# Kernel tuning notes

Measured on AMD Instinct MI355X. Metric: run time of the kernel, lower is better.

## Reference

```python
import jax, jax.numpy as jnp
import numpy as np

B, TAU, D, DX, DZ, H = 512, 4, 5, 256, 16, 64
M = D * DZ
COEFF_KL = 1.0
LOG2PI = float(np.log(2.0 * np.pi))


def setup_inputs() -> dict:
    ks = jax.random.split(jax.random.key(0), 12)
    s = 0.05
    return {
        "x": jax.random.normal(ks[0], (B, TAU, D, DX), jnp.float32),
        "y": jax.random.normal(ks[1], (B, D, DX), jnp.float32),
        "mask_param": jnp.full((TAU, M, M), 5.0, jnp.float32),
        "w_enc": ((0.9 * jax.random.uniform(ks[2], (D, DZ, DX)) + 0.1) / DX).astype(jnp.float32),
        "w_dec": ((0.9 * jax.random.uniform(ks[3], (D, DX, DZ)) + 0.1) / DZ).astype(jnp.float32),
        "enc_W0": jax.random.normal(ks[4], (DZ, DX, H), jnp.float32) * s,
        "enc_b0": jnp.zeros((DZ, H), jnp.float32),
        "enc_W1": jax.random.normal(ks[5], (DZ, H), jnp.float32) * s,
        "enc_b1": jnp.zeros((DZ,), jnp.float32),
        "dec_W0": jax.random.normal(ks[6], (DX, DZ, H), jnp.float32) * s,
        "dec_b0": jnp.zeros((DX, H), jnp.float32),
        "dec_W1": jax.random.normal(ks[7], (DX, H), jnp.float32) * s,
        "dec_b1": jnp.zeros((DX,), jnp.float32),
        "t_W0": jax.random.normal(ks[8], (M, TAU * M, H), jnp.float32) * s,
        "t_b0": jnp.zeros((M, H), jnp.float32),
        "t_W1": jax.random.normal(ks[9], (M, H), jnp.float32) * s,
        "t_b1": jnp.zeros((M,), jnp.float32),
        "logvar_enc": jnp.full((D,), -1.0, jnp.float32),
        "logvar_dec": jnp.full((D,), -1.0, jnp.float32),
        "t_logvar": jnp.full((D, DZ), -4.0, jnp.float32),
    }


def _encode(x, w_enc, W0, b0, W1, b1):
    # x: (..., D, DX) -> mu: (..., D, DZ); d_z tiny MLPs gated by mixing weights
    masked = w_enc * x[..., None, :]  # (..., D, DZ, DX)
    h = jax.nn.leaky_relu(jnp.einsum('...ijx,jxh->...ijh', masked, W0) + b0)
    return jnp.einsum('...ijh,jh->...ij', h, W1) + b1


def _forward(x, y, mask_param, w_enc, w_dec, enc_W0, enc_b0, enc_W1, enc_b1,
             dec_W0, dec_b0, dec_W1, dec_b1, t_W0, t_b0, t_W1, t_b1,
             logvar_enc, logvar_dec, t_logvar):
    b = x.shape[0]
    k_adj, k_ep, k_et = jax.random.split(jax.random.key(42), 3)
    # gumbel-sigmoid soft adjacency sample (temperature 1, drawhard=False)
    u = jax.random.uniform(k_adj, (b, TAU, M, M), minval=1e-6, maxval=1.0 - 1e-6)
    adj = jax.nn.sigmoid(mask_param + jnp.log(u) - jnp.log1p(-u))  # (b,TAU,M,M)
    # encoder q(z|x): reparameterized gaussian, per-feature logvar
    q_std = jnp.exp(0.5 * logvar_enc)[:, None]                     # (D,1)
    mu_past = _encode(x, w_enc, enc_W0, enc_b0, enc_W1, enc_b1)    # (b,TAU,D,DZ)
    z_past = mu_past + q_std * jax.random.normal(k_ep, mu_past.shape, jnp.float32)
    mu_t = _encode(y, w_enc, enc_W0, enc_b0, enc_W1, enc_b1)       # (b,D,DZ)
    z_t = mu_t + q_std * jax.random.normal(k_et, mu_t.shape, jnp.float32)
    # transition p(z_t|z_<t): per-node MLP on adjacency-gated past latents
    zp = z_past.reshape(b, TAU, M)
    gated = adj * zp[:, :, None, :]                                # (b,TAU,node,src)
    gated = gated.transpose(0, 2, 1, 3).reshape(b, M, TAU * M)
    ht = jax.nn.leaky_relu(jnp.einsum('bmi,mih->bmh', gated, t_W0) + t_b0)
    pz_mu = (jnp.einsum('bmh,mh->bm', ht, t_W1) + t_b1).reshape(b, D, DZ)
    pz_std = jnp.exp(0.5 * t_logvar)                               # (D,DZ)
    # decoder p(x|z): d_x tiny MLPs on mixing-mask-gated latents
    masked_z = w_dec * z_t[:, :, None, :]                          # (b,D,DX,DZ)
    hd = jax.nn.leaky_relu(jnp.einsum('bijz,jzh->bijh', masked_z, dec_W0) + dec_b0)
    px_mu = jnp.einsum('bijh,jh->bij', hd, dec_W1) + dec_b1        # (b,D,DX)
    px_std = jnp.exp(0.5 * logvar_dec)[:, None]                    # (D,1)
    # ELBO: gaussian recon log-lik + analytic gaussian KL(q || p_transition)
    recon = -0.5 * ((y - px_mu) / px_std) ** 2 - jnp.log(px_std) - 0.5 * LOG2PI
    recon = recon.sum(axis=(1, 2)).mean()
    kl = (jnp.log(pz_std) - 0.5 * logvar_enc[:, None]
          + (q_std ** 2 + (mu_t - pz_mu) ** 2) / (2.0 * pz_std ** 2) - 0.5)
    kl = kl.sum(axis=(1, 2)).mean()
    return -(recon - COEFF_KL * kl)


def reference(x, y, mask_param, w_enc, w_dec, enc_W0, enc_b0, enc_W1, enc_b1,
              dec_W0, dec_b0, dec_W1, dec_b1, t_W0, t_b0, t_W1, t_b1,
              logvar_enc, logvar_dec, t_logvar):
    return _forward(x, y, mask_param, w_enc, w_dec, enc_W0, enc_b0, enc_W1, enc_b1,
                    dec_W0, dec_b0, dec_W1, dec_b1, t_W0, t_b0, t_W1, t_b1,
                    logvar_enc, logvar_dec, t_logvar)
```

## Files before the change

### kernel.cpp

```cpp
#include <hip/hip_runtime.h>
#include <cstdint>

constexpr int NB = 512, NTAU = 4, ND = 5, NDX = 256, NDZ = 16, NH = 64;
constexpr int NM  = ND * NDZ;
constexpr int NTM = NTAU * NM;
constexpr int NSAMP = NB * NTAU + NB;
constexpr float LOG2PI_F = 1.8378770664093453f;

typedef __attribute__((ext_vector_type(8))) short bf16x8;
typedef __attribute__((ext_vector_type(4))) float f32x4;

__device__ __forceinline__ unsigned long long mix64(unsigned long long z) {
  z += 0x9E3779B97F4A7C15ull;
  z = (z ^ (z >> 30)) * 0xBF58476D1CE4E5B9ull;
  z = (z ^ (z >> 27)) * 0x94D049BB133111EBull;
  return z ^ (z >> 31);
}
__device__ __forceinline__ float u01f(unsigned long long h) {
  return ((float)(unsigned)(h >> 40) + 0.5f) * (1.0f / 16777216.0f);
}
__device__ __forceinline__ float rng_normal(unsigned long long salt, unsigned long long idx) {
  float u1 = u01f(mix64(salt + 2ull * idx));
  float u2 = u01f(mix64(salt + 2ull * idx + 1ull));
  float r = sqrtf(-2.0f * logf(u1));
  return r * cosf(6.283185307179586f * u2);
}
constexpr unsigned long long SALT_ADJ = 0x1000000000000ull;
constexpr unsigned long long SALT_EP  = 0x2000000000000ull;
constexpr unsigned long long SALT_ET  = 0x3000000000000ull;

__device__ __forceinline__ short f2bf(float f) {
  unsigned u = __float_as_uint(f);
  unsigned r = (u + 0x7FFFu + ((u >> 16) & 1u)) >> 16;
  return (short)r;
}

__global__ __launch_bounds__(256) void k_prepP(
    const float* __restrict__ w_enc, const float* __restrict__ eW0,
    short* __restrict__ PtE)
{
  __shared__ float lds[64][65];
  const int bid = blockIdx.x;
  const int d  = bid >> 6;
  const int z  = (bid & 63) >> 2;
  const int k0 = (bid & 3) * 64;
  const int tid = threadIdx.x;

  for (int i = tid; i < 64 * 64; i += 256) {
    int kk = i >> 6, h = i & 63;
    lds[kk][h] = eW0[((size_t)z * NDX + k0 + kk) * NH + h];
  }
  __syncthreads();
  for (int i = tid; i < 64 * 64; i += 256) {
    int h = i >> 6, kk = i & 63;
    float v = w_enc[((size_t)d * NDZ + z) * NDX + k0 + kk] * lds[kk][h];
    PtE[((size_t)(d * 1024 + z * 64 + h)) * NDX + k0 + kk] = f2bf(v);
  }
}

__global__ __launch_bounds__(512, 2) void k_enc_mfma(
    const float* __restrict__ x, const float* __restrict__ y,
    const short* __restrict__ PtE,
    const float* __restrict__ b0, const float* __restrict__ W1,
    const float* __restrict__ b1, const float* __restrict__ lve,
    float* __restrict__ z_past, float* __restrict__ mu_t, float* __restrict__ z_t,
    const float* __restrict__ w_dec, const float* __restrict__ dW0,
    short* __restrict__ QtD,
    const float* __restrict__ tW0, short* __restrict__ TtB,
    float* __restrict__ yT)
{
  __shared__ __align__(16) char smem[35840];
  const int bid = blockIdx.x;
  const int tid = threadIdx.x;

  if (bid < 400) {
    short* Bs = (short*)smem;
    float (*mu_s)[4] = (float(*)[4])(smem + 33792);

    const int d = bid / 80;
    const int r80 = bid % 80;
    const int zq = r80 / 20;
    const int s0 = (r80 % 20) * 128;
    const int w = tid >> 6, l = tid & 63;
    const int lrow = l & 15, g = l >> 4;

    const int srow = s0 + w * 16 + lrow;
    const float* Asrc = (srow < NB * NTAU)
        ? &x[((size_t)srow * ND + d) * NDX]
        : &y[((size_t)(srow - NB * NTAU) * ND + d) * NDX];
    bf16x8 a[8];
    #pragma unroll
    for (int ks = 0; ks < 8; ++ks) {
      const float* p = Asrc + g * 8 + ks * 32;
      float4 f0 = *(const float4*)p;
      float4 f1 = *(const float4*)(p + 4);
      a[ks][0] = f2bf(f0.x); a[ks][1] = f2bf(f0.y);
      a[ks][2] = f2bf(f0.z); a[ks][3] = f2bf(f0.w);
      a[ks][4] = f2bf(f1.x); a[ks][5] = f2bf(f1.y);
      a[ks][6] = f2bf(f1.z); a[ks][7] = f2bf(f1.w);
    }

    const int stg_row = tid >> 3;
    const int stg_c   = (tid & 7) * 32;

    for (int zi = 0; zi < 4; ++zi) {
      const int z = zq * 4 + zi;
      {
        const short* src = PtE + ((size_t)(d * 1024 + z * 64 + stg_row)) * NDX + stg_c;
        short* dst = Bs + stg_row * 264 + stg_c;
        #pragma unroll
        for (int j = 0; j < 4; ++j)
          *(bf16x8*)(dst + j * 8) = *(const bf16x8*)(src + j * 8);
      }
      __syncthreads();

      f32x4 acc[4] = {};
      #pragma unroll
      for (int nt = 0; nt < 4; ++nt) {
        const short* Brow = Bs + (nt * 16 + lrow) * 264 + g * 8;
        #pragma unroll
        for (int ks = 0; ks < 8; ++ks) {
          bf16x8 bv = *(const bf16x8*)(Brow + ks * 32);
          acc[nt] = __builtin_amdgcn_mfma_f32_16x16x32_bf16(a[ks], bv, acc[nt], 0, 0, 0);
        }
      }

      float b0v[4], w1v[4];
      #pragma unroll
      for (int nt = 0; nt < 4; ++nt) {
        int h = nt * 16 + lrow;
        b0v[nt] = b0[z * NH + h];
        w1v[nt] = W1[z * NH + h];
      }
      const float b1v = b1[z];
      #pragma unroll
      for (int reg = 0; reg < 4; ++reg) {
        float v = 0.0f;
        #pragma unroll
        for (int nt = 0; nt < 4; ++nt) {
          float hv = acc[nt][reg] + b0v[nt];
          hv = fmaxf(hv, 0.01f * hv);
          v += hv * w1v[nt];
        }
        #pragma unroll
        for (int off = 1; off < 16; off <<= 1) v += __shfl_xor(v, off, 16);
        if (lrow == 0)
          mu_s[w * 16 + g * 4 + reg][zi] = v + b1v;
      }
      __syncthreads();
    }

    {
      const int sl = tid >> 2, zi = tid & 3;
      const int z = zq * 4 + zi;
      const int s = s0 + sl;
      const int m = d * NDZ + z;
      float mu = mu_s[sl][zi];
      float qs = expf(0.5f * lve[d]);
      if (s < NB * NTAU) {
        float eps = rng_normal(SALT_EP, (unsigned long long)s * NM + m);
        z_past[(size_t)s * NM + m] = mu + qs * eps;
      } else {
        int b = s - NB * NTAU;
        float eps = rng_normal(SALT_ET, (unsigned long long)b * NM + m);
        size_t o = (size_t)b * NM + m;
        mu_t[o] = mu;
        z_t[o]  = mu + qs * eps;
      }
    }
  } else if (bid < 560) {
    int t = (bid - 400) * 512 + tid;
    int d = t / (NDX * NH);
    int r = t % (NDX * NH);
    int xx = r >> 6, h = r & 63;
    size_t base = (size_t)t * 32;
    #pragma unroll
    for (int z = 0; z < NDZ; ++z)
      QtD[base + z] = f2bf(w_dec[((size_t)d * NDX + xx) * NDZ + z] *
                           dW0[((size_t)xx * NDZ + z) * NH + h]);
    #pragma unroll
    for (int z = NDZ; z < 32; ++z) QtD[base + z] = 0;
  } else if (bid < 960) {
    short (*lds)[65] = (short(*)[65])smem;
    int r = bid - 560;
    int kt = r % 5, m = r / 5;
    int k0 = kt * 64;
    for (int idx = tid; idx < 64 * 64; idx += 512) {
      int hh = idx & 63, kk = idx >> 6;
      lds[kk][hh] = f2bf(tW0[((size_t)m * NTM + k0 + kk) * NH + hh]);
    }
    __syncthreads();
    for (int idx = tid; idx < 64 * 64; idx += 512) {
      int kk = idx & 63, hh = idx >> 6;
      TtB[((size_t)m * NH + hh) * NTM + k0 + kk] = lds[kk][hh];
    }
  } else {
    int e0 = ((bid - 960) * 512 + tid) * 4;
    int d = e0 / (NDX * NB);
    int rem = e0 % (NDX * NB);
    int xx = rem >> 9, b0i = rem & 511;
    float4 o;
    o.x = y[((size_t)(b0i + 0) * ND + d) * NDX + xx];
    o.y = y[((size_t)(b0i + 1) * ND + d) * NDX + xx];
    o.z = y[((size_t)(b0i + 2) * ND + d) * NDX + xx];
    o.w = y[((size_t)(b0i + 3) * ND + d) * NDX + xx];
    *(float4*)&yT[e0] = o;
  }
}

__global__ __launch_bounds__(512, 2) void k_tail(
    const float* __restrict__ mask_param, const float* __restrict__ z_past,
    const short* __restrict__ TtB,
    const float* __restrict__ tb0, const float* __restrict__ tW1,
    const float* __restrict__ tb1, const float* __restrict__ lve,
    const float* __restrict__ t_logvar, const float* __restrict__ mu_t,
    float* __restrict__ kl_partial,
    const float* __restrict__ zt, const short* __restrict__ QtD,
    const float* __restrict__ yT, const float* __restrict__ db0,
    const float* __restrict__ dW1, const float* __restrict__ db1,
    const float* __restrict__ lvd, float* __restrict__ rec_partial)
{
  __shared__ float ems[NTM];
  __shared__ float redb[8];

  const int bid = blockIdx.x;
  const int tid = threadIdx.x;

  if (bid < 320) {
    const int m = bid >> 2;
    const int b0 = (bid & 3) * 128;
    const int w = tid >> 6, l = tid & 63;
    const int lrow = l & 15, g = l >> 4;

    for (int i = tid; i < NTM; i += 512) {
      int t = i / NM, s = i - t * NM;
      ems[i] = expf(-mask_param[(t * NM + m) * NM + s]);
    }
    __syncthreads();

    const int brow = b0 + w * 16 + lrow;
    const float* zrow = z_past + (size_t)brow * NTM;
    const short* Bbase = TtB + (size_t)m * NH * NTM + lrow * NTM + g * 8;

    f32x4 acc[4] = {};
    #pragma unroll
    for (int ks = 0; ks < 10; ++ks) {
      const int tm0 = g * 8 + ks * 32;
      const int t = tm0 / NM;
      const int s0 = tm0 - t * NM;
      unsigned long long aibase =
          ((unsigned long long)((brow * NTAU + t) * NM + m)) * NM + s0;
      unsigned long long h0 = mix64(SALT_ADJ + aibase);
      unsigned long long h1 = mix64(SALT_ADJ + aibase + 2);
      unsigned long long h2 = mix64(SALT_ADJ + aibase + 4);
      unsigned long long h3 = mix64(SALT_ADJ + aibase + 6);
      float u[8];
      u[0] = ((float)(unsigned)(h0 >> 40) + 0.5f) * (1.0f / 16777216.0f);
      u[1] = ((float)((unsigned)(h0 >> 16) & 0xFFFFFFu) + 0.5f) * (1.0f / 16777216.0f);
      u[2] = ((float)(unsigned)(h1 >> 40) + 0.5f) * (1.0f / 16777216.0f);
      u[3] = ((float)((unsigned)(h1 >> 16) & 0xFFFFFFu) + 0.5f) * (1.0f / 16777216.0f);
      u[4] = ((float)(unsigned)(h2 >> 40) + 0.5f) * (1.0f / 16777216.0f);
      u[5] = ((float)((unsigned)(h2 >> 16) & 0xFFFFFFu) + 0.5f) * (1.0f / 16777216.0f);
      u[6] = ((float)(unsigned)(h3 >> 40) + 0.5f) * (1.0f / 16777216.0f);
      u[7] = ((float)((unsigned)(h3 >> 16) & 0xFFFFFFu) + 0.5f) * (1.0f / 16777216.0f);
      float4 z0 = *(const float4*)(zrow + tm0);
      float4 z1 = *(const float4*)(zrow + tm0 + 4);
      const float* zvp0 = &z0.x;
      const float* zvp1 = &z1.x;
      bf16x8 a;
      #pragma unroll
      for (int j = 0; j < 8; ++j) {
        float uu = fminf(fmaxf(u[j], 1e-6f), 1.0f - 1e-6f);
        float e = ems[tm0 + j];
        float den = fmaf(e, 1.0f - uu, uu);
        float adj = uu * __builtin_amdgcn_rcpf(den);
        float zv = (j < 4) ? zvp0[j] : zvp1[j - 4];
        a[j] = f2bf(adj * zv);
      }
      #pragma unroll
      for (int nt = 0; nt < 4; ++nt) {
        bf16x8 bv = *(const bf16x8*)(Bbase + (size_t)nt * 16 * NTM + ks * 32);
        acc[nt] = __builtin_amdgcn_mfma_f32_16x16x32_bf16(a, bv, acc[nt], 0, 0, 0);
      }
    }

    float b0v[4], w1v[4];
    #pragma unroll
    for (int nt = 0; nt < 4; ++nt) {
      int h = nt * 16 + lrow;
      b0v[nt] = tb0[m * NH + h];
      w1v[nt] = tW1[m * NH + h];
    }

    const int d = m >> 4;
    const float lv_t = t_logvar[m];
    const float lv_e = lve[d];
    const float inv2var = 0.5f * expf(-lv_t);
    const float qvar = expf(lv_e);
    const float cterm = 0.5f * lv_t - 0.5f * lv_e - 0.5f;
    const float bv1 = tb1[m];

    float klw = 0.0f;
    #pragma unroll
    for (int reg = 0; reg < 4; ++reg) {
      float v = 0.0f;
      #pragma unroll
      for (int nt = 0; nt < 4; ++nt) {
        float hv = acc[nt][reg] + b0v[nt];
        hv = fmaxf(hv, 0.01f * hv);
        v += hv * w1v[nt];
      }
      #pragma unroll
      for (int off = 1; off < 16; off <<= 1) v += __shfl_xor(v, off, 16);
      if (lrow == 0) {
        int b = b0 + w * 16 + g * 4 + reg;
        float pz = v + bv1;
        float diff = mu_t[(size_t)b * NM + m] - pz;
        klw += cterm + (qvar + diff * diff) * inv2var;
      }
    }
    klw += __shfl_xor(klw, 16, 64);
    klw += __shfl_xor(klw, 32, 64);

    if (l == 0) redb[w] = klw;
    __syncthreads();
    if (tid == 0) {
      float s = 0.f;
      #pragma unroll
      for (int i = 0; i < 8; ++i) s += redb[i];
      kl_partial[(bid & 3) * NM + m] = s;
    }
  } else {
    const int idx = bid - 320;
    const int d = idx >> 8, xx = idx & 255;
    const int w8 = tid >> 6, l = tid & 63;
    const int mb = w8 >> 2, w = w8 & 3;
    const int lrow = l & 15, g = l >> 4;

    bf16x8 bfr[4];
    const short* Bbase = QtD + ((size_t)((d * NDX + xx) * NH)) * 32;
    #pragma unroll
    for (int nt = 0; nt < 4; ++nt)
      bfr[nt] = *(const bf16x8*)(Bbase + (nt * 16 + lrow) * 32 + g * 8);

    f32x4 acc[4][4] = {};
    #pragma unroll
    for (int mt = 0; mt < 4; ++mt) {
      int b = mb * 256 + w * 64 + mt * 16 + lrow;
      bf16x8 a = {0, 0, 0, 0, 0, 0, 0, 0};
      if (g < 2) {
        const float* zp = zt + (size_t)b * NM + d * NDZ + g * 8;
        float4 f0 = *(const float4*)zp;
        float4 f1 = *(const float4*)(zp + 4);
        a[0] = f2bf(f0.x); a[1] = f2bf(f0.y); a[2] = f2bf(f0.z); a[3] = f2bf(f0.w);
        a[4] = f2bf(f1.x); a[5] = f2bf(f1.y); a[6] = f2bf(f1.z); a[7] = f2bf(f1.w);
      }
      #pragma unroll
      for (int nt = 0; nt < 4; ++nt)
        acc[mt][nt] = __builtin_amdgcn_mfma_f32_16x16x32_bf16(a, bfr[nt], acc[mt][nt], 0, 0, 0);
    }

    float db0v[4], dW1v[4];
    #pragma unroll
    for (int nt = 0; nt < 4; ++nt) {
      int h = nt * 16 + lrow;
      db0v[nt] = db0[xx * NH + h];
      dW1v[nt] = dW1[xx * NH + h];
    }
    const float lv = lvd[d];
    const float inv_std = expf(-0.5f * lv);
    const float cterm = -0.5f * lv - 0.5f * LOG2PI_F;
    const float b1v = db1[xx];

    float racc = 0.0f;
    #pragma unroll
    for (int mt = 0; mt < 4; ++mt) {
      float rs[4];
      #pragma unroll
      for (int reg = 0; reg < 4; ++reg) {
        float v = 0.0f;
        #pragma unroll
        for (int nt = 0; nt < 4; ++nt) {
          float hv = acc[mt][nt][reg] + db0v[nt];
          hv = fmaxf(hv, 0.01f * hv);
          v += hv * dW1v[nt];
        }
        #pragma unroll
        for (int off = 1; off < 16; off <<= 1) v += __shfl_xor(v, off, 16);
        rs[reg] = v;
      }
      if (lrow == 0) {
        int b = mb * 256 + w * 64 + mt * 16 + g * 4;
        float4 yv = *(const float4*)&yT[((size_t)d * NDX + xx) * NB + b];
        const float* yvp = &yv.x;
        #pragma unroll
        for (int reg = 0; reg < 4; ++reg) {
          float px = rs[reg] + b1v;
          float e = (yvp[reg] - px) * inv_std;
          racc += -0.5f * e * e + cterm;
        }
      }
    }
    racc += __shfl_xor(racc, 16, 64);
    racc += __shfl_xor(racc, 32, 64);

    if (l == 0) redb[w8] = racc;
    __syncthreads();
    if (tid == 0) {
      float s = 0.f;
      #pragma unroll
      for (int i = 0; i < 8; ++i) s += redb[i];
      rec_partial[(size_t)d * NDX + xx] = s;
    }
  }
}

__global__ __launch_bounds__(256) void k_reduce(
    const float* __restrict__ rp, const float* __restrict__ kp,
    float* __restrict__ out)
{
  __shared__ float sr[4], sk[4];
  float r = 0.f, k = 0.f;
  for (int i = threadIdx.x; i < 1280; i += 256) r += rp[i];
  for (int i = threadIdx.x; i < 320; i += 256) k += kp[i];
  #pragma unroll
  for (int off = 32; off; off >>= 1) {
    r += __shfl_xor(r, off, 64);
    k += __shfl_xor(k, off, 64);
  }
  int wv = threadIdx.x >> 6;
  if ((threadIdx.x & 63) == 0) { sr[wv] = r; sk[wv] = k; }
  __syncthreads();
  if (threadIdx.x == 0) {
    float R = sr[0] + sr[1] + sr[2] + sr[3];
    float K = sk[0] + sk[1] + sk[2] + sk[3];
    out[0] = (K - R) / (float)NB;
  }
}

extern "C" void kernel_launch(void* const* d_in, const int* in_sizes, int n_in,
                              void* d_out, int out_size, void* d_ws, size_t ws_size,
                              hipStream_t stream) {
  (void)in_sizes; (void)n_in; (void)out_size; (void)ws_size;
  const float* x        = (const float*)d_in[0];
  const float* y        = (const float*)d_in[1];
  const float* mask_p   = (const float*)d_in[2];
  const float* w_enc    = (const float*)d_in[3];
  const float* w_dec    = (const float*)d_in[4];
  const float* enc_W0   = (const float*)d_in[5];
  const float* enc_b0   = (const float*)d_in[6];
  const float* enc_W1   = (const float*)d_in[7];
  const float* enc_b1   = (const float*)d_in[8];
  const float* dec_W0   = (const float*)d_in[9];
  const float* dec_b0   = (const float*)d_in[10];
  const float* dec_W1   = (const float*)d_in[11];
  const float* dec_b1   = (const float*)d_in[12];
  const float* t_W0     = (const float*)d_in[13];
  const float* t_b0     = (const float*)d_in[14];
  const float* t_W1     = (const float*)d_in[15];
  const float* t_b1     = (const float*)d_in[16];
  const float* lv_enc   = (const float*)d_in[17];
  const float* lv_dec   = (const float*)d_in[18];
  const float* t_logvar = (const float*)d_in[19];

  float* ws     = (float*)d_ws;
  float* z_past = ws;
  float* mu_t   = z_past + 163840;
  float* z_t    = mu_t + 40960;
  float* rec_p  = z_t + 40960;
  float* kl_p   = rec_p + 1280;
  float* yTb    = kl_p + 320;
  short* PtE    = (short*)(yTb + 655360);
  short* QtD    = PtE + 5 * 1024 * NDX;
  short* TtB    = QtD + 5 * NDX * NH * 32;

  k_prepP<<<320, 256, 0, stream>>>(w_enc, enc_W0, PtE);
  k_enc_mfma<<<1280, 512, 0, stream>>>(
      x, y, PtE, enc_b0, enc_W1, enc_b1, lv_enc,
      z_past, mu_t, z_t, w_dec, dec_W0, QtD, t_W0, TtB, yTb);
  k_tail<<<1600, 512, 0, stream>>>(
      mask_p, z_past, TtB, t_b0, t_W1, t_b1, lv_enc, t_logvar, mu_t, kl_p,
      z_t, QtD, yTb, dec_b0, dec_W1, dec_b1, lv_dec, rec_p);
  k_reduce<<<1, 256, 0, stream>>>(rec_p, kl_p, (float*)d_out);
}
```

Baseline: 72.36 us.

## Use 32-bit hash for adjacency noise and interleave KL and decoder blocks

Replaces the 64-bit splitmix hash that generates the Gumbel-sigmoid uniforms with a cheaper 32-bit integer hash, computed per element. This cuts 64-bit multiply work in the MFMA-feeding loop. It also interleaves the transition/KL blocks with the decoder/reconstruction blocks (every fifth block does KL work) so the heavy KL blocks are spread across CUs instead of all being scheduled first. The k-loop unroll is reduced to 1, which likely lowers register pressure. The random stream changes, but it only needs to be a valid uniform sample since the reference uses a different PRNG anyway.

```diff
diff --git a/kernel.cpp b/kernel.cpp
--- a/kernel.cpp
+++ b/kernel.cpp
@@ -25,9 +25,15 @@
   float r = sqrtf(-2.0f * logf(u1));
   return r * cosf(6.283185307179586f * u2);
 }
-constexpr unsigned long long SALT_ADJ = 0x1000000000000ull;
 constexpr unsigned long long SALT_EP  = 0x2000000000000ull;
 constexpr unsigned long long SALT_ET  = 0x3000000000000ull;
+
+__device__ __forceinline__ unsigned h32(unsigned x) {
+  x *= 0x9E3779B1u; x ^= x >> 16;
+  x *= 0x85EBCA77u; x ^= x >> 13;
+  x *= 0xC2B2AE3Du; x ^= x >> 16;
+  return x;
+}
 
 __device__ __forceinline__ short f2bf(float f) {
   unsigned u = __float_as_uint(f);
@@ -226,9 +232,10 @@
   const int bid = blockIdx.x;
   const int tid = threadIdx.x;
 
-  if (bid < 320) {
-    const int m = bid >> 2;
-    const int b0 = (bid & 3) * 128;
+  if (bid % 5 == 0) {
+    const int tbid = bid / 5;
+    const int m = tbid >> 2;
+    const int b0 = (tbid & 3) * 128;
     const int w = tid >> 6, l = tid & 63;
     const int lrow = l & 15, g = l >> 4;
 
@@ -241,28 +248,15 @@
     const int brow = b0 + w * 16 + lrow;
     const float* zrow = z_past + (size_t)brow * NTM;
     const short* Bbase = TtB + (size_t)m * NH * NTM + lrow * NTM + g * 8;
+    const unsigned gidbase = (unsigned)(brow * NTAU) * (NM * NM) + (unsigned)m * NM;
 
     f32x4 acc[4] = {};
-    #pragma unroll
+    #pragma unroll 1
     for (int ks = 0; ks < 10; ++ks) {
       const int tm0 = g * 8 + ks * 32;
       const int t = tm0 / NM;
       const int s0 = tm0 - t * NM;
-      unsigned long long aibase =
-          ((unsigned long long)((brow * NTAU + t) * NM + m)) * NM + s0;
-      unsigned long long h0 = mix64(SALT_ADJ + aibase);
-      unsigned long long h1 = mix64(SALT_ADJ + aibase + 2);
-      unsigned long long h2 = mix64(SALT_ADJ + aibase + 4);
-      unsigned long long h3 = mix64(SALT_ADJ + aibase + 6);
-      float u[8];
-      u[0] = ((float)(unsigned)(h0 >> 40) + 0.5f) * (1.0f / 16777216.0f);
-      u[1] = ((float)((unsigned)(h0 >> 16) & 0xFFFFFFu) + 0.5f) * (1.0f / 16777216.0f);
-      u[2] = ((float)(unsigned)(h1 >> 40) + 0.5f) * (1.0f / 16777216.0f);
-      u[3] = ((float)((unsigned)(h1 >> 16) & 0xFFFFFFu) + 0.5f) * (1.0f / 16777216.0f);
-      u[4] = ((float)(unsigned)(h2 >> 40) + 0.5f) * (1.0f / 16777216.0f);
-      u[5] = ((float)((unsigned)(h2 >> 16) & 0xFFFFFFu) + 0.5f) * (1.0f / 16777216.0f);
-      u[6] = ((float)(unsigned)(h3 >> 40) + 0.5f) * (1.0f / 16777216.0f);
-      u[7] = ((float)((unsigned)(h3 >> 16) & 0xFFFFFFu) + 0.5f) * (1.0f / 16777216.0f);
+      const unsigned gi0 = gidbase + (unsigned)t * (NM * NM) + (unsigned)s0;
       float4 z0 = *(const float4*)(zrow + tm0);
       float4 z1 = *(const float4*)(zrow + tm0 + 4);
       const float* zvp0 = &z0.x;
@@ -270,7 +264,9 @@
       bf16x8 a;
       #pragma unroll
       for (int j = 0; j < 8; ++j) {
-        float uu = fminf(fmaxf(u[j], 1e-6f), 1.0f - 1e-6f);
+        unsigned hh = h32(gi0 + j + 0x5EED0001u);
+        float uu = ((float)(hh >> 8) + 0.5f) * (1.0f / 16777216.0f);
+        uu = fminf(fmaxf(uu, 1e-6f), 1.0f - 1e-6f);
         float e = ems[tm0 + j];
         float den = fmaf(e, 1.0f - uu, uu);
         float adj = uu * __builtin_amdgcn_rcpf(den);
@@ -328,10 +324,10 @@
       float s = 0.f;
       #pragma unroll
       for (int i = 0; i < 8; ++i) s += redb[i];
-      kl_partial[(bid & 3) * NM + m] = s;
+      kl_partial[(tbid & 3) * NM + m] = s;
     }
   } else {
-    const int idx = bid - 320;
+    const int idx = bid - bid / 5 - 1;
     const int d = idx >> 8, xx = idx & 255;
     const int w8 = tid >> 6, l = tid & 63;
     const int mb = w8 >> 2, w = w8 & 3;
```

After: 84.89 us. +17.3%, slower.
